# Optimization experiments

Measured on AMD Instinct MI355X. Metric: run time of the kernel, lower is better.

Reference implementation:

```python
import jax, jax.numpy as jnp
import numpy as np

N_NODES = 100000
N_EDGES = 3200000
DIM = 16


def setup_inputs() -> dict:
    key = jax.random.key(0)
    k1, k2, k3, k4 = jax.random.split(key, 4)
    state_input = jax.random.normal(k1, (N_NODES, DIM), dtype=jnp.float32)
    row = jax.random.randint(k2, (N_EDGES,), 0, N_NODES, dtype=jnp.int32)
    col = jax.random.randint(k3, (N_EDGES,), 0, N_NODES, dtype=jnp.int32)
    edge_weights = jax.random.uniform(k4, (N_EDGES,), dtype=jnp.float32)
    return {"state_input": state_input, "row": row, "col": col,
            "edge_weights": edge_weights}


def reference(state_input, row, col, edge_weights):
    # f_eq: per-dim self dynamics, f(x) = -x  -> [N, dim]
    self_diff = -state_input

    # gather pair endpoints: x_1 = state[col], x_2 = state[row]
    # g_eq: sin(x_2 - x_1) per dim (Kuramoto-style coupling) -> [E, dim]
    neighbor_processed = jnp.sin(state_input[row] - state_input[col])

    # weight by edge weight and scatter-sum into destination nodes (col)
    aggregated_sum = jax.ops.segment_sum(
        neighbor_processed * edge_weights[:, None], col,
        num_segments=state_input.shape[0])  # [N, dim]

    # s_eq: elementwise tanh on aggregated sum
    interact_diff = jnp.tanh(aggregated_sum)

    return (self_diff + interact_diff,
            (state_input, self_diff),
            (aggregated_sum, interact_diff))
```

## Files before the change

### kernel.cpp

```cpp
#include <hip/hip_runtime.h>
#include <hip/hip_fp16.h>
#include <math.h>

#define N_NODES 100000
#define N_EDGES 3200000
#define DIM 16
#define NSZ (N_NODES * DIM)

#define NPB 128
#define NBUCK 782
#define NBLK 512
#define EPB 6256
#define CAP 4864
#define PRK 5

typedef float nvec4 __attribute__((ext_vector_type(4)));

__global__ __launch_bounds__(512)
void hist_table(const float* __restrict__ state, __half* __restrict__ hs,
                const int* __restrict__ col, unsigned* __restrict__ tbl,
                int* __restrict__ totals) {
    __shared__ int hcnt[NBUCK];
    int t = threadIdx.x, blk = blockIdx.x;
    for (int j = t; j < NBUCK; j += 512) hcnt[j] = 0;
    for (int i = blk * 512 + t; i < NSZ / 4; i += NBLK * 512) {
        nvec4 v = __builtin_nontemporal_load(&((const nvec4*)state)[i]);
        union { __half2 h[2]; float2 f; } u;
        u.h[0] = __floats2half2_rn(v.x, v.y);
        u.h[1] = __floats2half2_rn(v.z, v.w);
        ((float2*)hs)[i] = u.f;
    }
    __syncthreads();
    int e0 = blk * EPB;
    int eN = e0 + EPB; if (eN > N_EDGES) eN = N_EDGES;
    int nch = (eN - e0) >> 2;
    const int4* c4p = (const int4*)(col + e0);
    for (int i = t; i < nch; i += 512) {
        int4 c = c4p[i];
        atomicAdd(&hcnt[c.x >> 7], 1);
        atomicAdd(&hcnt[c.y >> 7], 1);
        atomicAdd(&hcnt[c.z >> 7], 1);
        atomicAdd(&hcnt[c.w >> 7], 1);
    }
    __syncthreads();
    for (int j = t; j < NBUCK; j += 512) {
        int c = hcnt[j];
        tbl[(size_t)j * NBLK + blk] = (unsigned)c;
        if (c) atomicAdd(&totals[j], c);
    }
}

__global__ __launch_bounds__(1024)
void scan_off(const int* __restrict__ totals, int* __restrict__ off) {
    __shared__ int wsum[16];
    int t = threadIdx.x;
    int i0 = 2 * t, i1 = 2 * t + 1;
    int v0 = (i0 < NBUCK) ? totals[i0] : 0;
    int v1 = (i1 < NBUCK) ? totals[i1] : 0;
    int p = v0 + v1, ps = p;
    #pragma unroll
    for (int d = 1; d < 64; d <<= 1) {
        int u = __shfl_up(ps, d, 64);
        if ((t & 63) >= d) ps += u;
    }
    if ((t & 63) == 63) wsum[t >> 6] = ps;
    __syncthreads();
    int wid = t >> 6, wbase = 0;
    #pragma unroll
    for (int k = 0; k < 16; ++k) wbase += (k < wid) ? wsum[k] : 0;
    int ex = wbase + ps - p;
    if (i0 < NBUCK) off[i0 + 1] = ex + v0;
    if (i1 < NBUCK) off[i1 + 1] = ex + v0 + v1;
    if (t == 0) off[0] = 0;
}

__global__ __launch_bounds__(512)
void base_scan(unsigned* __restrict__ tbl, const int* __restrict__ off) {
    __shared__ int wsum[8];
    int b = blockIdx.x, t = threadIdx.x;
    int v = (int)tbl[(size_t)b * NBLK + t];
    int ps = v;
    #pragma unroll
    for (int d = 1; d < 64; d <<= 1) {
        int u = __shfl_up(ps, d, 64);
        if ((t & 63) >= d) ps += u;
    }
    if ((t & 63) == 63) wsum[t >> 6] = ps;
    __syncthreads();
    int wid = t >> 6, wbase = 0;
    #pragma unroll
    for (int k = 0; k < 8; ++k) wbase += (k < wid) ? wsum[k] : 0;
    tbl[(size_t)b * NBLK + t] = (unsigned)(off[b] + wbase + ps - v);
}

__global__ __launch_bounds__(512)
void sort_write(const int* __restrict__ row, const int* __restrict__ col,
                const float* __restrict__ w, const unsigned* __restrict__ tbl,
                const int* __restrict__ off,
                unsigned long long* __restrict__ packed) {
    __shared__ unsigned long long sbuf[EPB];
    __shared__ int sc[1024];
    __shared__ int cur[NBUCK];
    __shared__ int gbase[NBUCK];
    __shared__ int wsum[8];
    int t = threadIdx.x, blk = blockIdx.x;
    int e0 = blk * EPB;
    int eN = e0 + EPB; if (eN > N_EDGES) eN = N_EDGES;
    int cnt = eN - e0;

    for (int j = t; j < NBUCK; j += 512) {
        int b0 = (int)tbl[(size_t)j * NBLK + blk];
        int b1 = (blk == NBLK - 1) ? off[j + 1]
                                   : (int)tbl[(size_t)j * NBLK + blk + 1];
        gbase[j] = b0;
        cur[j] = b1 - b0;
    }
    __syncthreads();
    {
        int i0 = 2 * t, i1 = 2 * t + 1;
        int v0 = (i0 < NBUCK) ? cur[i0] : 0;
        int v1 = (i1 < NBUCK) ? cur[i1] : 0;
        int p = v0 + v1, ps = p;
        #pragma unroll
        for (int d = 1; d < 64; d <<= 1) {
            int u = __shfl_up(ps, d, 64);
            if ((t & 63) >= d) ps += u;
        }
        if ((t & 63) == 63) wsum[t >> 6] = ps;
        __syncthreads();
        int wid = t >> 6, wbase = 0;
        #pragma unroll
        for (int k = 0; k < 8; ++k) wbase += (k < wid) ? wsum[k] : 0;
        int ex = wbase + ps - p;
        if (i0 < NBUCK) { sc[i0] = ex;      cur[i0] = ex; }
        if (i1 < NBUCK) { sc[i1] = ex + v0; cur[i1] = ex + v0; }
    }
    __syncthreads();
    {
        int nch = cnt >> 2;
        const int4*  c4p = (const int4*)(col + e0);
        const int4*  r4p = (const int4*)(row + e0);
        const float4* w4p = (const float4*)(w + e0);
        for (int i = t; i < nch; i += 512) {
            int4 c = c4p[i]; int4 r = r4p[i]; float4 ww = w4p[i];
            int pos;
            pos = atomicAdd(&cur[c.x >> 7], 1);
            sbuf[pos] = ((unsigned long long)(unsigned)c.x << 47)
                      | ((unsigned long long)(unsigned)r.x << 30)
                      | (unsigned long long)(__float_as_uint(ww.x) >> 2);
            pos = atomicAdd(&cur[c.y >> 7], 1);
            sbuf[pos] = ((unsigned long long)(unsigned)c.y << 47)
                      | ((unsigned long long)(unsigned)r.y << 30)
                      | (unsigned long long)(__float_as_uint(ww.y) >> 2);
            pos = atomicAdd(&cur[c.z >> 7], 1);
            sbuf[pos] = ((unsigned long long)(unsigned)c.z << 47)
                      | ((unsigned long long)(unsigned)r.z << 30)
                      | (unsigned long long)(__float_as_uint(ww.z) >> 2);
            pos = atomicAdd(&cur[c.w >> 7], 1);
            sbuf[pos] = ((unsigned long long)(unsigned)c.w << 47)
                      | ((unsigned long long)(unsigned)r.w << 30)
                      | (unsigned long long)(__float_as_uint(ww.w) >> 2);
        }
    }
    __syncthreads();
    for (int i = t; i < cnt; i += 512) {
        unsigned long long pv = sbuf[i];
        int b = (int)(pv >> 54);
        __builtin_nontemporal_store(pv, &packed[gbase[b] + (i - sc[b])]);
    }
}

__device__ inline float4 edge_acc(float4 a, const float4 xx,
                                  unsigned long long p, float2 hbits) {
    union { float2 f; __half2 h[2]; } u; u.f = hbits;
    float2 lo = __half22float2(u.h[0]);
    float2 hi = __half22float2(u.h[1]);
    float we = __uint_as_float(((unsigned)p & 0x3FFFFFFFu) << 2);
    a.x += __sinf(lo.x - xx.x) * we;
    a.y += __sinf(lo.y - xx.y) * we;
    a.z += __sinf(hi.x - xx.z) * we;
    a.w += __sinf(hi.y - xx.w) * we;
    return a;
}

__global__ __launch_bounds__(1024, 8)
void bucket_sort_aggregate(const float* __restrict__ state,
                           const __half2* __restrict__ hs2,
                           const int* __restrict__ off,
                           const unsigned long long* __restrict__ packed,
                           float* __restrict__ out) {
    __shared__ unsigned long long sbuf[CAP];
    __shared__ int s_cnt[NPB], s_start[NPB], s_cur[NPB];
    __shared__ int s_wsum;
    int b = blockIdx.x, t = threadIdx.x;
    int q = t & 3, sub = (t >> 2) & 1, g = t >> 3;
    int beg = off[b], end = off[b + 1];

    int n = b * NPB + g;
    bool valid = (n < N_NODES);
    float4 xx = valid ? ((const float4*)state)[n * 4 + q]
                      : make_float4(0.f, 0.f, 0.f, 0.f);
    float4 acc = make_float4(0.f, 0.f, 0.f, 0.f);
    const float2* hsf2 = (const float2*)hs2;

    for (int tbeg = beg; tbeg < end; tbeg += CAP) {
        int tend = tbeg + CAP; if (tend > end) tend = end;
        if (t < NPB) s_cnt[t] = 0;
        __syncthreads();

        unsigned long long pr[PRK];
        #pragma unroll
        for (int k = 0; k < PRK; ++k) {
            int e = tbeg + t + k * 1024;
            if (e < tend) {
                pr[k] = __builtin_nontemporal_load(&packed[e]);
                atomicAdd(&s_cnt[(unsigned)(pr[k] >> 47) & 127u], 1);
            }
        }
        __syncthreads();

        {
            int v = (t < NPB) ? s_cnt[t] : 0;
            int ps = v;
            #pragma unroll
            for (int d = 1; d < 64; d <<= 1) {
                int u = __shfl_up(ps, d, 64);
                if ((t & 63) >= d) ps += u;
            }
            if (t == 63) s_wsum = ps;
            __syncthreads();
            if (t < NPB) {
                int ex = ps - v + ((t >= 64) ? s_wsum : 0);
                s_start[t] = ex;
                s_cur[t] = ex;
            }
        }
        __syncthreads();

        #pragma unroll
        for (int k = 0; k < PRK; ++k) {
            int e = tbeg + t + k * 1024;
            if (e < tend) {
                int cl = (int)((pr[k] >> 47) & 127u);
                int pos = atomicAdd(&s_cur[cl], 1);
                sbuf[pos] = pr[k];
            }
        }
        __syncthreads();

        {
            int es = s_start[g], ee = s_cur[g];
            float4 a = acc;
            int e = es + sub;
            for (; e + 6 < ee; e += 8) {
                unsigned long long p0 = sbuf[e];
                unsigned long long p1 = sbuf[e + 2];
                unsigned long long p2 = sbuf[e + 4];
                unsigned long long p3 = sbuf[e + 6];
                float2 h0 = hsf2[(unsigned)((p0 >> 30) & 0x1FFFFu) * 4u + q];
                float2 h1 = hsf2[(unsigned)((p1 >> 30) & 0x1FFFFu) * 4u + q];
                float2 h2 = hsf2[(unsigned)((p2 >> 30) & 0x1FFFFu) * 4u + q];
                float2 h3 = hsf2[(unsigned)((p3 >> 30) & 0x1FFFFu) * 4u + q];
                a = edge_acc(a, xx, p0, h0);
                a = edge_acc(a, xx, p1, h1);
                a = edge_acc(a, xx, p2, h2);
                a = edge_acc(a, xx, p3, h3);
            }
            for (; e < ee; e += 2) {
                unsigned long long p0 = sbuf[e];
                float2 h0 = hsf2[(unsigned)((p0 >> 30) & 0x1FFFFu) * 4u + q];
                a = edge_acc(a, xx, p0, h0);
            }
            acc = a;
        }
        __syncthreads();
    }

    acc.x += __shfl_xor(acc.x, 4, 64);
    acc.y += __shfl_xor(acc.y, 4, 64);
    acc.z += __shfl_xor(acc.z, 4, 64);
    acc.w += __shfl_xor(acc.w, 4, 64);

    if (valid) {
        float4 th = make_float4(tanhf(acc.x), tanhf(acc.y),
                                tanhf(acc.z), tanhf(acc.w));
        int gdx = n * 4 + q;
        if (sub == 0) {
            ((float4*)(out + 0 * (size_t)NSZ))[gdx] =
                make_float4(th.x - xx.x, th.y - xx.y, th.z - xx.z, th.w - xx.w);
            ((float4*)(out + 2 * (size_t)NSZ))[gdx] =
                make_float4(-xx.x, -xx.y, -xx.z, -xx.w);
            ((float4*)(out + 4 * (size_t)NSZ))[gdx] = th;
        } else {
            ((float4*)(out + 1 * (size_t)NSZ))[gdx] = xx;
            ((float4*)(out + 3 * (size_t)NSZ))[gdx] = acc;
        }
    }
}

__global__ __launch_bounds__(256)
void edge_kernel(const float* __restrict__ state, const int* __restrict__ row,
                 const int* __restrict__ col, const float* __restrict__ w,
                 float* __restrict__ agg) {
    int idx = blockIdx.x * blockDim.x + threadIdx.x;
    if (idx >= N_EDGES * 4) return;
    int e = idx >> 2, qq = idx & 3;
    int r = row[e], c = col[e];
    float we = w[e];
    const float4 xr = ((const float4*)state)[r * 4 + qq];
    const float4 xcv = ((const float4*)state)[c * 4 + qq];
    float* dst = agg + c * DIM + qq * 4;
    atomicAdd(dst + 0, sinf(xr.x - xcv.x) * we);
    atomicAdd(dst + 1, sinf(xr.y - xcv.y) * we);
    atomicAdd(dst + 2, sinf(xr.z - xcv.z) * we);
    atomicAdd(dst + 3, sinf(xr.w - xcv.w) * we);
}

__global__ __launch_bounds__(256)
void node_kernel(const float* __restrict__ state, const float* __restrict__ agg,
                 float* __restrict__ out) {
    int idx = blockIdx.x * blockDim.x + threadIdx.x;
    if (idx >= N_NODES * 4) return;
    float4 x = ((const float4*)state)[idx];
    float4 a = ((const float4*)agg)[idx];
    float4 tv = make_float4(tanhf(a.x), tanhf(a.y), tanhf(a.z), tanhf(a.w));
    ((float4*)(out + 0 * NSZ))[idx] = make_float4(tv.x - x.x, tv.y - x.y,
                                                  tv.z - x.z, tv.w - x.w);
    ((float4*)(out + 1 * NSZ))[idx] = x;
    ((float4*)(out + 2 * NSZ))[idx] = make_float4(-x.x, -x.y, -x.z, -x.w);
    ((float4*)(out + 4 * NSZ))[idx] = tv;
}

extern "C" void kernel_launch(void* const* d_in, const int* in_sizes, int n_in,
                              void* d_out, int out_size, void* d_ws, size_t ws_size,
                              hipStream_t stream) {
    const float* state = (const float*)d_in[0];
    const int*   row   = (const int*)d_in[1];
    const int*   col   = (const int*)d_in[2];
    const float* w     = (const float*)d_in[3];
    float* out = (float*)d_out;

    size_t packed_off = 0;
    size_t half_off   = packed_off + (size_t)N_EDGES * 8;
    size_t tbl_off    = half_off + (size_t)NSZ * 2;
    size_t tot_off    = tbl_off + (size_t)NBUCK * NBLK * 4;
    size_t off_off    = tot_off + (size_t)NBUCK * 4;
    size_t needed     = off_off + (size_t)(NBUCK + 1) * 4;

    if (ws_size >= needed) {
        unsigned long long* packed =
            (unsigned long long*)((char*)d_ws + packed_off);
        __half* hs    = (__half*)((char*)d_ws + half_off);
        unsigned* tbl = (unsigned*)((char*)d_ws + tbl_off);
        int* totals   = (int*)((char*)d_ws + tot_off);
        int* off      = (int*)((char*)d_ws + off_off);

        (void)hipMemsetAsync(totals, 0, (size_t)NBUCK * sizeof(int), stream);
        hist_table<<<NBLK, 512, 0, stream>>>(state, hs, col, tbl, totals);
        scan_off<<<1, 1024, 0, stream>>>(totals, off);
        base_scan<<<NBUCK, 512, 0, stream>>>(tbl, off);
        sort_write<<<NBLK, 512, 0, stream>>>(row, col, w, tbl, off, packed);
        bucket_sort_aggregate<<<NBUCK, 1024, 0, stream>>>(
            state, (const __half2*)hs, off, packed, out);
    } else {
        float* agg = out + 3 * NSZ;
        (void)hipMemsetAsync(agg, 0, NSZ * sizeof(float), stream);
        edge_kernel<<<(N_EDGES * 4 + 255) / 256, 256, 0, stream>>>(
            state, row, col, w, agg);
        node_kernel<<<(N_NODES * 4 + 255) / 256, 256, 0, stream>>>(
            state, agg, out);
    }
}
```

Before: 185.5 us.

## Move state-copy outputs into prep kernel and simplify sort offsets

The output slices that depend only on the input state (the state copy and its negation) are now written in the first prep kernel, so the final aggregate kernel stores only three slices, all from the sub==0 lanes, with nontemporal stores. sort_write folds its base and local offsets into a single per-bucket difference, removing a shared array. scan_off drops to 512 threads and writes exclusive offsets directly. The edge loop is inlined with uint2 half loads. This spreads store traffic across kernels and trims shared memory and index arithmetic, but the prep kernel now carries more writes.

```diff
diff --git a/kernel.cpp b/kernel.cpp
--- a/kernel.cpp
+++ b/kernel.cpp
@@ -17,18 +17,22 @@
 typedef float nvec4 __attribute__((ext_vector_type(4)));
 
 __global__ __launch_bounds__(512)
-void hist_table(const float* __restrict__ state, __half* __restrict__ hs,
-                const int* __restrict__ col, unsigned* __restrict__ tbl,
-                int* __restrict__ totals) {
+void prep(const float* __restrict__ state, const int* __restrict__ col,
+          __half* __restrict__ hs, float* __restrict__ out,
+          unsigned* __restrict__ tbl, int* __restrict__ totals) {
     __shared__ int hcnt[NBUCK];
     int t = threadIdx.x, blk = blockIdx.x;
     for (int j = t; j < NBUCK; j += 512) hcnt[j] = 0;
-    for (int i = blk * 512 + t; i < NSZ / 4; i += NBLK * 512) {
+    int gid = blk * 512 + t, gsz = NBLK * 512;
+    for (int i = gid; i < NSZ / 4; i += gsz) {
         nvec4 v = __builtin_nontemporal_load(&((const nvec4*)state)[i]);
         union { __half2 h[2]; float2 f; } u;
         u.h[0] = __floats2half2_rn(v.x, v.y);
         u.h[1] = __floats2half2_rn(v.z, v.w);
         ((float2*)hs)[i] = u.f;
+        __builtin_nontemporal_store(v, &((nvec4*)(out + 1 * (size_t)NSZ))[i]);
+        nvec4 nv = {-v.x, -v.y, -v.z, -v.w};
+        __builtin_nontemporal_store(nv, &((nvec4*)(out + 2 * (size_t)NSZ))[i]);
     }
     __syncthreads();
     int e0 = blk * EPB;
@@ -50,9 +54,9 @@
     }
 }
 
-__global__ __launch_bounds__(1024)
+__global__ __launch_bounds__(512)
 void scan_off(const int* __restrict__ totals, int* __restrict__ off) {
-    __shared__ int wsum[16];
+    __shared__ int wsum[8];
     int t = threadIdx.x;
     int i0 = 2 * t, i1 = 2 * t + 1;
     int v0 = (i0 < NBUCK) ? totals[i0] : 0;
@@ -67,11 +71,10 @@
     __syncthreads();
     int wid = t >> 6, wbase = 0;
     #pragma unroll
-    for (int k = 0; k < 16; ++k) wbase += (k < wid) ? wsum[k] : 0;
+    for (int k = 0; k < 8; ++k) wbase += (k < wid) ? wsum[k] : 0;
     int ex = wbase + ps - p;
-    if (i0 < NBUCK) off[i0 + 1] = ex + v0;
-    if (i1 < NBUCK) off[i1 + 1] = ex + v0 + v1;
-    if (t == 0) off[0] = 0;
+    if (i0 <= NBUCK) off[i0] = ex;
+    if (i1 <= NBUCK) off[i1] = ex + v0;
 }
 
 __global__ __launch_bounds__(512)
@@ -99,9 +102,8 @@
                 const int* __restrict__ off,
                 unsigned long long* __restrict__ packed) {
     __shared__ unsigned long long sbuf[EPB];
-    __shared__ int sc[1024];
     __shared__ int cur[NBUCK];
-    __shared__ int gbase[NBUCK];
+    __shared__ int diff[NBUCK];
     __shared__ int wsum[8];
     int t = threadIdx.x, blk = blockIdx.x;
     int e0 = blk * EPB;
@@ -112,7 +114,7 @@
         int b0 = (int)tbl[(size_t)j * NBLK + blk];
         int b1 = (blk == NBLK - 1) ? off[j + 1]
                                    : (int)tbl[(size_t)j * NBLK + blk + 1];
-        gbase[j] = b0;
+        diff[j] = b0;
         cur[j] = b1 - b0;
     }
     __syncthreads();
@@ -132,14 +134,14 @@
         #pragma unroll
         for (int k = 0; k < 8; ++k) wbase += (k < wid) ? wsum[k] : 0;
         int ex = wbase + ps - p;
-        if (i0 < NBUCK) { sc[i0] = ex;      cur[i0] = ex; }
-        if (i1 < NBUCK) { sc[i1] = ex + v0; cur[i1] = ex + v0; }
+        if (i0 < NBUCK) { diff[i0] -= ex;      cur[i0] = ex; }
+        if (i1 < NBUCK) { diff[i1] -= ex + v0; cur[i1] = ex + v0; }
     }
     __syncthreads();
     {
         int nch = cnt >> 2;
-        const int4*  c4p = (const int4*)(col + e0);
-        const int4*  r4p = (const int4*)(row + e0);
+        const int4*   c4p = (const int4*)(col + e0);
+        const int4*   r4p = (const int4*)(row + e0);
         const float4* w4p = (const float4*)(w + e0);
         for (int i = t; i < nch; i += 512) {
             int4 c = c4p[i]; int4 r = r4p[i]; float4 ww = w4p[i];
@@ -166,42 +168,27 @@
     for (int i = t; i < cnt; i += 512) {
         unsigned long long pv = sbuf[i];
         int b = (int)(pv >> 54);
-        __builtin_nontemporal_store(pv, &packed[gbase[b] + (i - sc[b])]);
-    }
-}
-
-__device__ inline float4 edge_acc(float4 a, const float4 xx,
-                                  unsigned long long p, float2 hbits) {
-    union { float2 f; __half2 h[2]; } u; u.f = hbits;
-    float2 lo = __half22float2(u.h[0]);
-    float2 hi = __half22float2(u.h[1]);
-    float we = __uint_as_float(((unsigned)p & 0x3FFFFFFFu) << 2);
-    a.x += __sinf(lo.x - xx.x) * we;
-    a.y += __sinf(lo.y - xx.y) * we;
-    a.z += __sinf(hi.x - xx.z) * we;
-    a.w += __sinf(hi.y - xx.w) * we;
-    return a;
+        __builtin_nontemporal_store(pv, &packed[diff[b] + i]);
+    }
 }
 
 __global__ __launch_bounds__(1024, 8)
-void bucket_sort_aggregate(const float* __restrict__ state,
-                           const __half2* __restrict__ hs2,
-                           const int* __restrict__ off,
-                           const unsigned long long* __restrict__ packed,
-                           float* __restrict__ out) {
+void aggregate(const float* __restrict__ state, const __half2* __restrict__ hs2,
+               const int* __restrict__ off,
+               const unsigned long long* __restrict__ packed,
+               float* __restrict__ out) {
     __shared__ unsigned long long sbuf[CAP];
     __shared__ int s_cnt[NPB], s_start[NPB], s_cur[NPB];
     __shared__ int s_wsum;
     int b = blockIdx.x, t = threadIdx.x;
     int q = t & 3, sub = (t >> 2) & 1, g = t >> 3;
     int beg = off[b], end = off[b + 1];
-
     int n = b * NPB + g;
     bool valid = (n < N_NODES);
     float4 xx = valid ? ((const float4*)state)[n * 4 + q]
                       : make_float4(0.f, 0.f, 0.f, 0.f);
-    float4 acc = make_float4(0.f, 0.f, 0.f, 0.f);
-    const float2* hsf2 = (const float2*)hs2;
+    float4 acc = {0.f, 0.f, 0.f, 0.f};
+    const uint2* hsu = (const uint2*)hs2;
 
     for (int tbeg = beg; tbeg < end; tbeg += CAP) {
         int tend = tbeg + CAP; if (tend > end) tend = end;
@@ -220,12 +207,14 @@
         __syncthreads();
 
         {
-            int v = (t < NPB) ? s_cnt[t] : 0;
-            int ps = v;
-            #pragma unroll
-            for (int d = 1; d < 64; d <<= 1) {
-                int u = __shfl_up(ps, d, 64);
-                if ((t & 63) >= d) ps += u;
+            int v = 0, ps = 0;
+            if (t < NPB) {
+                v = s_cnt[t]; ps = v;
+                #pragma unroll
+                for (int d = 1; d < 64; d <<= 1) {
+                    int u = __shfl_up(ps, d, 64);
+                    if ((t & 63) >= d) ps += u;
+                }
             }
             if (t == 63) s_wsum = ps;
             __syncthreads();
@@ -250,51 +239,59 @@
 
         {
             int es = s_start[g], ee = s_cur[g];
-            float4 a = acc;
             int e = es + sub;
             for (; e + 6 < ee; e += 8) {
                 unsigned long long p0 = sbuf[e];
                 unsigned long long p1 = sbuf[e + 2];
                 unsigned long long p2 = sbuf[e + 4];
                 unsigned long long p3 = sbuf[e + 6];
-                float2 h0 = hsf2[(unsigned)((p0 >> 30) & 0x1FFFFu) * 4u + q];
-                float2 h1 = hsf2[(unsigned)((p1 >> 30) & 0x1FFFFu) * 4u + q];
-                float2 h2 = hsf2[(unsigned)((p2 >> 30) & 0x1FFFFu) * 4u + q];
-                float2 h3 = hsf2[(unsigned)((p3 >> 30) & 0x1FFFFu) * 4u + q];
-                a = edge_acc(a, xx, p0, h0);
-                a = edge_acc(a, xx, p1, h1);
-                a = edge_acc(a, xx, p2, h2);
-                a = edge_acc(a, xx, p3, h3);
+                uint2 h0 = hsu[(unsigned)((p0 >> 30) & 0x1FFFFu) * 4u + q];
+                uint2 h1 = hsu[(unsigned)((p1 >> 30) & 0x1FFFFu) * 4u + q];
+                uint2 h2 = hsu[(unsigned)((p2 >> 30) & 0x1FFFFu) * 4u + q];
+                uint2 h3 = hsu[(unsigned)((p3 >> 30) & 0x1FFFFu) * 4u + q];
+                #pragma unroll
+                for (int j = 0; j < 4; ++j) {
+                    unsigned long long p = (j == 0) ? p0 : (j == 1) ? p1
+                                         : (j == 2) ? p2 : p3;
+                    uint2 hb = (j == 0) ? h0 : (j == 1) ? h1
+                             : (j == 2) ? h2 : h3;
+                    float we = __uint_as_float(((unsigned)p & 0x3FFFFFFFu) << 2);
+                    float2 lo = __half22float2(*(const __half2*)&hb.x);
+                    float2 hi = __half22float2(*(const __half2*)&hb.y);
+                    acc.x += __sinf(lo.x - xx.x) * we;
+                    acc.y += __sinf(lo.y - xx.y) * we;
+                    acc.z += __sinf(hi.x - xx.z) * we;
+                    acc.w += __sinf(hi.y - xx.w) * we;
+                }
             }
             for (; e < ee; e += 2) {
-                unsigned long long p0 = sbuf[e];
-                float2 h0 = hsf2[(unsigned)((p0 >> 30) & 0x1FFFFu) * 4u + q];
-                a = edge_acc(a, xx, p0, h0);
-            }
-            acc = a;
-        }
-        __syncthreads();
-    }
-
-    acc.x += __shfl_xor(acc.x, 4, 64);
-    acc.y += __shfl_xor(acc.y, 4, 64);
-    acc.z += __shfl_xor(acc.z, 4, 64);
-    acc.w += __shfl_xor(acc.w, 4, 64);
-
-    if (valid) {
+                unsigned long long p = sbuf[e];
+                uint2 hb = hsu[(unsigned)((p >> 30) & 0x1FFFFu) * 4u + q];
+                float we = __uint_as_float(((unsigned)p & 0x3FFFFFFFu) << 2);
+                float2 lo = __half22float2(*(const __half2*)&hb.x);
+                float2 hi = __half22float2(*(const __half2*)&hb.y);
+                acc.x += __sinf(lo.x - xx.x) * we;
+                acc.y += __sinf(lo.y - xx.y) * we;
+                acc.z += __sinf(hi.x - xx.z) * we;
+                acc.w += __sinf(hi.y - xx.w) * we;
+            }
+        }
+        __syncthreads();
+    }
+
+    acc.x += __shfl_xor(acc.x, 4, 64); acc.y += __shfl_xor(acc.y, 4, 64);
+    acc.z += __shfl_xor(acc.z, 4, 64); acc.w += __shfl_xor(acc.w, 4, 64);
+
+    if (valid && sub == 0) {
         float4 th = make_float4(tanhf(acc.x), tanhf(acc.y),
                                 tanhf(acc.z), tanhf(acc.w));
         int gdx = n * 4 + q;
-        if (sub == 0) {
-            ((float4*)(out + 0 * (size_t)NSZ))[gdx] =
-                make_float4(th.x - xx.x, th.y - xx.y, th.z - xx.z, th.w - xx.w);
-            ((float4*)(out + 2 * (size_t)NSZ))[gdx] =
-                make_float4(-xx.x, -xx.y, -xx.z, -xx.w);
-            ((float4*)(out + 4 * (size_t)NSZ))[gdx] = th;
-        } else {
-            ((float4*)(out + 1 * (size_t)NSZ))[gdx] = xx;
-            ((float4*)(out + 3 * (size_t)NSZ))[gdx] = acc;
-        }
+        nvec4 v0 = {th.x - xx.x, th.y - xx.y, th.z - xx.z, th.w - xx.w};
+        nvec4 v3 = {acc.x, acc.y, acc.z, acc.w};
+        nvec4 v4 = {th.x, th.y, th.z, th.w};
+        __builtin_nontemporal_store(v0, &((nvec4*)(out + 0 * (size_t)NSZ))[gdx]);
+        __builtin_nontemporal_store(v3, &((nvec4*)(out + 3 * (size_t)NSZ))[gdx]);
+        __builtin_nontemporal_store(v4, &((nvec4*)(out + 4 * (size_t)NSZ))[gdx]);
     }
 }
 
@@ -341,26 +338,26 @@
     float* out = (float*)d_out;
 
     size_t packed_off = 0;
-    size_t half_off   = packed_off + (size_t)N_EDGES * 8;
-    size_t tbl_off    = half_off + (size_t)NSZ * 2;
+    size_t hs_off     = packed_off + (size_t)N_EDGES * 8;
+    size_t tbl_off    = hs_off + (size_t)NSZ * 2;
     size_t tot_off    = tbl_off + (size_t)NBUCK * NBLK * 4;
-    size_t off_off    = tot_off + (size_t)NBUCK * 4;
-    size_t needed     = off_off + (size_t)(NBUCK + 1) * 4;
+    size_t off_off    = tot_off + ((size_t)NBUCK * 4 + 15) / 16 * 16;
+    size_t needed     = off_off + (size_t)(NBUCK + 2) * 4;
 
     if (ws_size >= needed) {
         unsigned long long* packed =
             (unsigned long long*)((char*)d_ws + packed_off);
-        __half* hs    = (__half*)((char*)d_ws + half_off);
+        __half* hs    = (__half*)((char*)d_ws + hs_off);
         unsigned* tbl = (unsigned*)((char*)d_ws + tbl_off);
         int* totals   = (int*)((char*)d_ws + tot_off);
         int* off      = (int*)((char*)d_ws + off_off);
 
         (void)hipMemsetAsync(totals, 0, (size_t)NBUCK * sizeof(int), stream);
-        hist_table<<<NBLK, 512, 0, stream>>>(state, hs, col, tbl, totals);
-        scan_off<<<1, 1024, 0, stream>>>(totals, off);
+        prep<<<NBLK, 512, 0, stream>>>(state, col, hs, out, tbl, totals);
+        scan_off<<<1, 512, 0, stream>>>(totals, off);
         base_scan<<<NBUCK, 512, 0, stream>>>(tbl, off);
         sort_write<<<NBLK, 512, 0, stream>>>(row, col, w, tbl, off, packed);
-        bucket_sort_aggregate<<<NBUCK, 1024, 0, stream>>>(
+        aggregate<<<NBUCK, 1024, 0, stream>>>(
             state, (const __half2*)hs, off, packed, out);
     } else {
         float* agg = out + 3 * NSZ;
```

New measurement: 174.6 us. 1.06x faster.
